# Performance work log

Hardware: AMD Instinct MI355X
Metric: run time of the kernel (lower is better)

Reference implementation:

```python
import jax, jax.numpy as jnp
import numpy as np
import math

D_MODEL = 1024
N_HEADS = 16
SLOT_DIM = 64
N_SLOTS = 1024
TOP_K = 2
LN_EPS = 1e-5


def setup_inputs() -> dict:
    key = jax.random.key(0)
    ks = jax.random.split(key, 8)
    x = jax.random.normal(ks[0], (4, 2048, D_MODEL), dtype=jnp.float32)
    ln_gamma = jnp.ones((D_MODEL,), jnp.float32)
    ln_beta = jnp.zeros((D_MODEL,), jnp.float32)
    q_w = jax.random.normal(ks[1], (N_HEADS * SLOT_DIM, D_MODEL), jnp.float32) / math.sqrt(D_MODEL)
    q_b = jnp.zeros((N_HEADS * SLOT_DIM,), jnp.float32)
    slot_signatures = jax.random.normal(ks[2], (N_HEADS, N_SLOTS, SLOT_DIM), jnp.float32) * 0.5
    slot_values = jax.random.normal(ks[3], (N_HEADS, N_SLOTS, SLOT_DIM), jnp.float32) * 0.02
    out_w = jax.random.normal(ks[4], (D_MODEL, N_HEADS * SLOT_DIM), jnp.float32) / math.sqrt(N_HEADS * SLOT_DIM)
    out_b = jnp.zeros((D_MODEL,), jnp.float32)
    temperature = jnp.ones((1,), jnp.float32)
    return {"x": x, "ln_gamma": ln_gamma, "ln_beta": ln_beta, "q_w": q_w, "q_b": q_b,
            "slot_signatures": slot_signatures, "slot_values": slot_values,
            "out_w": out_w, "out_b": out_b, "temperature": temperature}


def _ternary_ste(sig):
    # forward = {-1,0,+1} quantization; backward = identity (straight-through)
    q = jnp.where(sig > 0.3, 1.0, jnp.where(sig < -0.3, -1.0, 0.0))
    return sig + jax.lax.stop_gradient(q - sig)


def reference(x, ln_gamma, ln_beta, q_w, q_b, slot_signatures, slot_values, out_w, out_b, temperature):
    B, T, D = x.shape
    # LayerNorm
    mean = jnp.mean(x, axis=-1, keepdims=True)
    var = jnp.var(x, axis=-1, keepdims=True)
    x_norm = (x - mean) * jax.lax.rsqrt(var + LN_EPS) * ln_gamma + ln_beta
    # Query projection -> [B, T, H, slot_dim]
    q = (x_norm @ q_w.T + q_b).reshape(B, T, N_HEADS, SLOT_DIM)
    sigs = _ternary_ste(slot_signatures)  # [H, S, d]
    scores = jnp.einsum('bthd,hsd->bths', q, sigs)
    scores = scores / (temperature * math.sqrt(SLOT_DIM))  # [B, T, H, S]
    # top-k routing
    topk_scores, slot_idx = jax.lax.top_k(scores, TOP_K)  # [B, T, H, K]
    weights = jax.nn.softmax(topk_scores, axis=-1)
    # gather selected slot values: [B, T, H, K, d]
    h_idx = jnp.arange(N_HEADS)[None, None, :, None]
    selected = slot_values[h_idx, slot_idx]
    read = jnp.sum(selected * weights[..., None], axis=3)  # [B, T, H, d]
    read = read.reshape(B, T, N_HEADS * SLOT_DIM)
    out = read @ out_w.T + out_b
    return x + out
```

## Files before the change

kernel.cpp:

```cpp
#include <hip/hip_runtime.h>

typedef unsigned short u16;
typedef unsigned int   u32;
typedef float f32x4  __attribute__((ext_vector_type(4)));
typedef float f32x16 __attribute__((ext_vector_type(16)));
typedef __bf16 bf16x8 __attribute__((ext_vector_type(8)));

__device__ __forceinline__ u16 f2bf(float f){
  u32 u = __float_as_uint(f);
  u += 0x7fffu + ((u >> 16) & 1u);
  return (u16)(u >> 16);
}

__device__ __forceinline__ void gld16(const void* g, void* l){
  __builtin_amdgcn_global_load_lds((const __attribute__((address_space(1))) u32*)g,
                                   (__attribute__((address_space(3))) u32*)l, 16, 0, 0);
}

__global__ __launch_bounds__(256) void convert_kernel(
    const float* __restrict__ qw, const float* __restrict__ ow,
    const float* __restrict__ sg,
    u16* __restrict__ qwb, u16* __restrict__ owb, u16* __restrict__ sgb){
  int i = (blockIdx.x * 256 + threadIdx.x) * 4;
  f32x4 a = *(const f32x4*)(qw + i);
  f32x4 b = *(const f32x4*)(ow + i);
  f32x4 s = *(const f32x4*)(sg + i);
  uint2 pa, pb, ps;
  pa.x = (u32)f2bf(a[0]) | ((u32)f2bf(a[1]) << 16);
  pa.y = (u32)f2bf(a[2]) | ((u32)f2bf(a[3]) << 16);
  pb.x = (u32)f2bf(b[0]) | ((u32)f2bf(b[1]) << 16);
  pb.y = (u32)f2bf(b[2]) | ((u32)f2bf(b[3]) << 16);
  float t0 = (s[0] > 0.3f) ? 1.0f : ((s[0] < -0.3f) ? -1.0f : 0.0f);
  float t1 = (s[1] > 0.3f) ? 1.0f : ((s[1] < -0.3f) ? -1.0f : 0.0f);
  float t2 = (s[2] > 0.3f) ? 1.0f : ((s[2] < -0.3f) ? -1.0f : 0.0f);
  float t3 = (s[3] > 0.3f) ? 1.0f : ((s[3] < -0.3f) ? -1.0f : 0.0f);
  ps.x = (u32)f2bf(t0) | ((u32)f2bf(t1) << 16);
  ps.y = (u32)f2bf(t2) | ((u32)f2bf(t3) << 16);
  *(uint2*)(qwb + i) = pa;
  *(uint2*)(owb + i) = pb;
  *(uint2*)(sgb + i) = ps;
}

__global__ __launch_bounds__(256) void ln_kernel(
    const float* __restrict__ x, const float* __restrict__ g,
    const float* __restrict__ b, u16* __restrict__ xn){
  const int t = blockIdx.x, tid = threadIdx.x;
  f32x4 v = *(const f32x4*)(x + (size_t)t * 1024 + tid * 4);
  float s  = v[0] + v[1] + v[2] + v[3];
  float ss = v[0]*v[0] + v[1]*v[1] + v[2]*v[2] + v[3]*v[3];
  for (int off = 32; off; off >>= 1){
    s  += __shfl_down(s, off);
    ss += __shfl_down(ss, off);
  }
  __shared__ float red[8];
  int w = tid >> 6;
  if ((tid & 63) == 0){ red[w] = s; red[4 + w] = ss; }
  __syncthreads();
  s  = red[0] + red[1] + red[2] + red[3];
  ss = red[4] + red[5] + red[6] + red[7];
  float mean = s * (1.0f / 1024.0f);
  float var  = ss * (1.0f / 1024.0f) - mean * mean;
  float rs   = rsqrtf(var + 1e-5f);
  f32x4 gv = *(const f32x4*)(g + tid * 4);
  f32x4 bv = *(const f32x4*)(b + tid * 4);
  float y0 = (v[0]-mean)*rs*gv[0]+bv[0];
  float y1 = (v[1]-mean)*rs*gv[1]+bv[1];
  float y2 = (v[2]-mean)*rs*gv[2]+bv[2];
  float y3 = (v[3]-mean)*rs*gv[3]+bv[3];
  uint2 pk;
  pk.x = (u32)f2bf(y0) | ((u32)f2bf(y1) << 16);
  pk.y = (u32)f2bf(y2) | ((u32)f2bf(y3) << 16);
  *(uint2*)(xn + (size_t)t * 1024 + tid * 4) = pk;
}

__global__ __launch_bounds__(256, 3) void gemm_bt(
    const u16* __restrict__ A, const u16* __restrict__ B,
    const float* __restrict__ bias, const float* __restrict__ resid,
    float* __restrict__ outf, u16* __restrict__ outb, int mode){
  __shared__ u16 As[128 * 64];
  __shared__ u16 Bs[128 * 64];
  const int tid = threadIdx.x;
  const int b = blockIdx.x;
  const int m0 = ((b & 7) * 8 + ((b >> 3) & 7)) * 128;
  const int n0 = (b >> 6) * 128;
  const int w = tid >> 6, lane = tid & 63, lm = lane & 15, quad = lane >> 4;
  const int wm = (w & 1) * 64, wn = (w >> 1) * 64;
  const int lr = lane >> 3;
  const int lg = (lane & 7) ^ lr;
  const f32x4 fz = {0.f, 0.f, 0.f, 0.f};
  f32x4 acc[4][4];
  #pragma unroll
  for (int i = 0; i < 4; ++i)
    #pragma unroll
    for (int j = 0; j < 4; ++j) acc[i][j] = fz;

  const u16* gA = A + (size_t)(m0 + w * 32 + lr) * 1024 + lg * 8;
  const u16* gB = B + (size_t)(n0 + w * 32 + lr) * 1024 + lg * 8;
  u16* lA = &As[(w * 32) * 64];
  u16* lB = &Bs[(w * 32) * 64];
  const int sw = lm & 7;

  for (int kt = 0; kt < 16; ++kt){
    #pragma unroll
    for (int sub = 0; sub < 4; ++sub){
      gld16(gA + (size_t)(sub * 8) * 1024 + kt * 64, lA + sub * 8 * 64);
      gld16(gB + (size_t)(sub * 8) * 1024 + kt * 64, lB + sub * 8 * 64);
    }
    __syncthreads();
    #pragma unroll
    for (int kk = 0; kk < 2; ++kk){
      const int ch = ((quad + kk * 4) ^ sw) * 8;
      bf16x8 afr[4], bfr[4];
      #pragma unroll
      for (int i = 0; i < 4; ++i)
        afr[i] = *(const bf16x8*)(&As[(wm + i * 16 + lm) * 64 + ch]);
      #pragma unroll
      for (int j = 0; j < 4; ++j)
        bfr[j] = *(const bf16x8*)(&Bs[(wn + j * 16 + lm) * 64 + ch]);
      #pragma unroll
      for (int i = 0; i < 4; ++i)
        #pragma unroll
        for (int j = 0; j < 4; ++j)
          acc[i][j] = __builtin_amdgcn_mfma_f32_16x16x32_bf16(afr[i], bfr[j], acc[i][j], 0, 0, 0);
    }
    __syncthreads();
  }

  #pragma unroll
  for (int i = 0; i < 4; ++i){
    #pragma unroll
    for (int r = 0; r < 4; ++r){
      int grow = m0 + wm + i * 16 + quad * 4 + r;
      #pragma unroll
      for (int j = 0; j < 4; ++j){
        int gcol = n0 + wn + j * 16 + lm;
        float v = acc[i][j][r] + bias[gcol];
        if (mode){
          v += resid[(size_t)grow * 1024 + gcol];
          outf[(size_t)grow * 1024 + gcol] = v;
        } else {
          outb[(size_t)grow * 1024 + gcol] = f2bf(v);
        }
      }
    }
  }
}

__global__ __launch_bounds__(256) void route_kernel(
    const u16* __restrict__ q, const u16* __restrict__ sig,
    const float* __restrict__ V, const float* __restrict__ temp,
    u16* __restrict__ rd){
  const int h = blockIdx.y;
  const int t0 = blockIdx.x * 128;
  const int tid = threadIdx.x, w = tid >> 6, lane = tid & 63;
  const int col = lane & 31, half = lane >> 5;

  __shared__ u16 sbuf[2][128 * 64];
  __shared__ float fw1[128], fw2[128];
  __shared__ int   fi1[128], fi2[128];

  const u16* qrow = q + (size_t)(t0 + w * 32 + col) * 1024 + h * 64 + half * 8;
  bf16x8 afr[4];
  #pragma unroll
  for (int c = 0; c < 4; ++c) afr[c] = *(const bf16x8*)(qrow + c * 16);

  const u16* sigh = sig + (size_t)h * 65536;

  const int lr = lane >> 3, lg = (lane & 7) ^ lr;
  const u16* ssrc = sigh + (size_t)(w * 32 + lr) * 64 + lg * 8;
  auto stage = [&](int t, int bb){
    const u16* s0 = ssrc + (size_t)t * 128 * 64;
    u16* d0 = &sbuf[bb][(w * 32) * 64];
    #pragma unroll
    for (int sub = 0; sub < 4; ++sub)
      gld16(s0 + sub * 8 * 64, d0 + sub * 8 * 64);
  };

  int p0 = ((0 + half) ^ (col & 7)) * 8;
  int p1 = ((2 + half) ^ (col & 7)) * 8;
  int p2 = ((4 + half) ^ (col & 7)) * 8;
  int p3 = ((6 + half) ^ (col & 7)) * 8;

  u32 rk[16];
  #pragma unroll
  for (int r = 0; r < 16; ++r) rk[r] = (u32)((r & 3) + 8 * (r >> 2) + 4 * half);

  const f32x16 fzero = {};
  float v1 = -3.0e38f, v2 = -3.0e38f;
  u32 b1 = 0, b2 = 0;

  stage(0, 0);
  for (int t = 0; t < 8; ++t){
    __syncthreads();
    if (t < 7) stage(t + 1, (t + 1) & 1);
    const u16* buf = sbuf[t & 1];
    #pragma unroll
    for (int sbl = 0; sbl < 4; ++sbl){
      const u16* srow = &buf[(sbl * 32 + col) * 64];
      bf16x8 s0 = *(const bf16x8*)(srow + p0);
      bf16x8 s1 = *(const bf16x8*)(srow + p1);
      bf16x8 s2 = *(const bf16x8*)(srow + p2);
      bf16x8 s3 = *(const bf16x8*)(srow + p3);
      f32x16 acc;
      acc = __builtin_amdgcn_mfma_f32_32x32x16_bf16(s0, afr[0], fzero, 0, 0, 0);
      acc = __builtin_amdgcn_mfma_f32_32x32x16_bf16(s1, afr[1], acc, 0, 0, 0);
      acc = __builtin_amdgcn_mfma_f32_32x32x16_bf16(s2, afr[2], acc, 0, 0, 0);
      acc = __builtin_amdgcn_mfma_f32_32x32x16_bf16(s3, afr[3], acc, 0, 0, 0);
      float k[16];
      #pragma unroll
      for (int r = 0; r < 16; ++r)
        k[r] = __uint_as_float((__float_as_uint(acc[r]) & 0xFFFFFFE0u) | rk[r]);
      float h1[8], h2[8];
      #pragma unroll
      for (int i = 0; i < 8; ++i){
        h1[i] = fmaxf(k[2*i], k[2*i+1]);
        h2[i] = fminf(k[2*i], k[2*i+1]);
      }
      float g1[4], g2[4];
      #pragma unroll
      for (int i = 0; i < 4; ++i){
        g1[i] = fmaxf(h1[2*i], h1[2*i+1]);
        g2[i] = __builtin_amdgcn_fmed3f(h1[2*i], h1[2*i+1], fmaxf(h2[2*i], h2[2*i+1]));
      }
      float e1[2], e2[2];
      #pragma unroll
      for (int i = 0; i < 2; ++i){
        e1[i] = fmaxf(g1[2*i], g1[2*i+1]);
        e2[i] = __builtin_amdgcn_fmed3f(g1[2*i], g1[2*i+1], fmaxf(g2[2*i], g2[2*i+1]));
      }
      float m1 = fmaxf(e1[0], e1[1]);
      float m2 = __builtin_amdgcn_fmed3f(e1[0], e1[1], fmaxf(e2[0], e2[1]));
      u32 bt = (u32)(t * 4 + sbl);
      u32   cb2 = (m2 > v2) ? bt : b2;
      float c2  = fmaxf(v2, m2);
      u32   nb1 = (m1 > v1) ? bt : b1;
      float n1  = fmaxf(v1, m1);
      float n2  = __builtin_amdgcn_fmed3f(v1, m1, c2);
      u32   nb2 = (n2 == m1) ? bt : ((n2 == v1) ? b1 : cb2);
      v1 = n1; b1 = nb1; v2 = n2; b2 = nb2;
    }
  }

  {
    float o1 = __shfl_xor(v1, 32);
    float o2 = __shfl_xor(v2, 32);
    u32 ob1 = (u32)__shfl_xor((int)b1, 32);
    u32 ob2 = (u32)__shfl_xor((int)b2, 32);
    u32   cb2 = (o2 > v2) ? ob2 : b2;
    float c2  = fmaxf(v2, o2);
    u32   nb1 = (o1 > v1) ? ob1 : b1;
    float n1  = fmaxf(v1, o1);
    float n2  = __builtin_amdgcn_fmed3f(v1, o1, c2);
    u32   nb2 = (n2 == o1) ? ob1 : ((n2 == v1) ? b1 : cb2);
    v1 = n1; b1 = nb1; v2 = n2; b2 = nb2;
  }

  if (half == 0){
    int tl = w * 32 + col;
    u32 u1 = __float_as_uint(v1);
    u32 u2 = __float_as_uint(v2);
    float s1 = __uint_as_float(u1 & 0xFFFFFFE0u);
    float s2 = __uint_as_float(u2 & 0xFFFFFFE0u);
    float tsc = 1.0f / (temp[0] * 8.0f);
    float ex = __expf((s2 - s1) * tsc);
    float iw = 1.0f / (1.0f + ex);
    fw1[tl] = iw; fw2[tl] = ex * iw;
    fi1[tl] = (int)(b1 * 32 + (u1 & 31u));
    fi2[tl] = (int)(b2 * 32 + (u2 & 31u));
  }
  __syncthreads();

  int tl = tid >> 1, d0 = (tid & 1) * 32;
  const float* va = V + ((size_t)h * 1024 + fi1[tl]) * 64 + d0;
  const float* vb = V + ((size_t)h * 1024 + fi2[tl]) * 64 + d0;
  float W1 = fw1[tl], W2 = fw2[tl];
  u16* dst = rd + (size_t)(t0 + tl) * 1024 + h * 64 + d0;
  #pragma unroll
  for (int g = 0; g < 4; ++g){
    f32x4 xa = *(const f32x4*)(va + g * 8);
    f32x4 xb = *(const f32x4*)(va + g * 8 + 4);
    f32x4 ya = *(const f32x4*)(vb + g * 8);
    f32x4 yb = *(const f32x4*)(vb + g * 8 + 4);
    uint4 o;
    o.x = (u32)f2bf(W1*xa[0]+W2*ya[0]) | ((u32)f2bf(W1*xa[1]+W2*ya[1]) << 16);
    o.y = (u32)f2bf(W1*xa[2]+W2*ya[2]) | ((u32)f2bf(W1*xa[3]+W2*ya[3]) << 16);
    o.z = (u32)f2bf(W1*xb[0]+W2*yb[0]) | ((u32)f2bf(W1*xb[1]+W2*yb[1]) << 16);
    o.w = (u32)f2bf(W1*xb[2]+W2*yb[2]) | ((u32)f2bf(W1*xb[3]+W2*yb[3]) << 16);
    *(uint4*)(dst + g * 8) = o;
  }
}

extern "C" void kernel_launch(void* const* d_in, const int* in_sizes, int n_in,
                              void* d_out, int out_size, void* d_ws, size_t ws_size,
                              hipStream_t stream){
  const float* x    = (const float*)d_in[0];
  const float* lng  = (const float*)d_in[1];
  const float* lnb  = (const float*)d_in[2];
  const float* qw   = (const float*)d_in[3];
  const float* qb   = (const float*)d_in[4];
  const float* sig  = (const float*)d_in[5];
  const float* sv   = (const float*)d_in[6];
  const float* ow   = (const float*)d_in[7];
  const float* ob   = (const float*)d_in[8];
  const float* temp = (const float*)d_in[9];
  float* out = (float*)d_out;

  char* ws = (char*)d_ws;
  u16* xn   = (u16*)(ws);
  u16* qwb  = (u16*)(ws + 16777216);
  u16* owb  = (u16*)(ws + 16777216 + 2097152);
  u16* sgb  = (u16*)(ws + 16777216 + 2 * 2097152);
  u16* qb16 = (u16*)(ws + 16777216 + 3 * 2097152);
  u16* rdb  = xn;

  convert_kernel<<<1024, 256, 0, stream>>>(qw, ow, sig, qwb, owb, sgb);
  ln_kernel<<<8192, 256, 0, stream>>>(x, lng, lnb, xn);
  gemm_bt<<<512, 256, 0, stream>>>(xn, qwb, qb, nullptr, nullptr, qb16, 0);
  route_kernel<<<dim3(64, 16), 256, 0, stream>>>(qb16, sgb, sv, temp, rdb);
  gemm_bt<<<512, 256, 0, stream>>>(rdb, owb, ob, x, out, nullptr, 1);
}
```

Baseline: 211.7 us.

## Double-buffer GEMM LDS tiles and switch routing scores to 16x16 MFMA

The GEMM kernel now double-buffers its A/B LDS tiles, issuing the next K-tile's global-to-LDS loads before computing the current one and dropping the trailing barrier. This doubles LDS use and lowers the occupancy hint from 3 to 2 blocks. The routing kernel replaces its 32x32x16 MFMA score computation with 16x16x32 MFMAs over two token sets per wave. It packs a 4-bit slot index into the score mantissa instead of 5 bits and adds a two-stage shuffle reduction across quads. The aim is to hide load latency in the GEMM and shorten the top-2 reduction chain, at the cost of slightly more index-packing truncation of scores.

```diff
diff --git a/kernel.cpp b/kernel.cpp
--- a/kernel.cpp
+++ b/kernel.cpp
@@ -3,7 +3,6 @@
 typedef unsigned short u16;
 typedef unsigned int   u32;
 typedef float f32x4  __attribute__((ext_vector_type(4)));
-typedef float f32x16 __attribute__((ext_vector_type(16)));
 typedef __bf16 bf16x8 __attribute__((ext_vector_type(8)));
 
 __device__ __forceinline__ u16 f2bf(float f){
@@ -73,12 +72,12 @@
   *(uint2*)(xn + (size_t)t * 1024 + tid * 4) = pk;
 }
 
-__global__ __launch_bounds__(256, 3) void gemm_bt(
+__global__ __launch_bounds__(256, 2) void gemm_bt(
     const u16* __restrict__ A, const u16* __restrict__ B,
     const float* __restrict__ bias, const float* __restrict__ resid,
     float* __restrict__ outf, u16* __restrict__ outb, int mode){
-  __shared__ u16 As[128 * 64];
-  __shared__ u16 Bs[128 * 64];
+  __shared__ u16 As[2][128 * 64];
+  __shared__ u16 Bs[2][128 * 64];
   const int tid = threadIdx.x;
   const int b = blockIdx.x;
   const int m0 = ((b & 7) * 8 + ((b >> 3) & 7)) * 128;
@@ -96,34 +95,39 @@
 
   const u16* gA = A + (size_t)(m0 + w * 32 + lr) * 1024 + lg * 8;
   const u16* gB = B + (size_t)(n0 + w * 32 + lr) * 1024 + lg * 8;
-  u16* lA = &As[(w * 32) * 64];
-  u16* lB = &Bs[(w * 32) * 64];
+  const int lbase = (w * 32) * 64;
   const int sw = lm & 7;
 
+  auto stage = [&](int kt, int bb){
+    #pragma unroll
+    for (int sub = 0; sub < 4; ++sub){
+      gld16(gA + (size_t)(sub * 8) * 1024 + kt * 64, &As[bb][lbase + sub * 8 * 64]);
+      gld16(gB + (size_t)(sub * 8) * 1024 + kt * 64, &Bs[bb][lbase + sub * 8 * 64]);
+    }
+  };
+
+  stage(0, 0);
   for (int kt = 0; kt < 16; ++kt){
-    #pragma unroll
-    for (int sub = 0; sub < 4; ++sub){
-      gld16(gA + (size_t)(sub * 8) * 1024 + kt * 64, lA + sub * 8 * 64);
-      gld16(gB + (size_t)(sub * 8) * 1024 + kt * 64, lB + sub * 8 * 64);
-    }
     __syncthreads();
+    if (kt < 15) stage(kt + 1, (kt + 1) & 1);
+    const u16* as = As[kt & 1];
+    const u16* bs = Bs[kt & 1];
     #pragma unroll
     for (int kk = 0; kk < 2; ++kk){
       const int ch = ((quad + kk * 4) ^ sw) * 8;
       bf16x8 afr[4], bfr[4];
       #pragma unroll
       for (int i = 0; i < 4; ++i)
-        afr[i] = *(const bf16x8*)(&As[(wm + i * 16 + lm) * 64 + ch]);
+        afr[i] = *(const bf16x8*)(&as[(wm + i * 16 + lm) * 64 + ch]);
       #pragma unroll
       for (int j = 0; j < 4; ++j)
-        bfr[j] = *(const bf16x8*)(&Bs[(wn + j * 16 + lm) * 64 + ch]);
+        bfr[j] = *(const bf16x8*)(&bs[(wn + j * 16 + lm) * 64 + ch]);
       #pragma unroll
       for (int i = 0; i < 4; ++i)
         #pragma unroll
         for (int j = 0; j < 4; ++j)
           acc[i][j] = __builtin_amdgcn_mfma_f32_16x16x32_bf16(afr[i], bfr[j], acc[i][j], 0, 0, 0);
     }
-    __syncthreads();
   }
 
   #pragma unroll
@@ -153,16 +157,17 @@
   const int h = blockIdx.y;
   const int t0 = blockIdx.x * 128;
   const int tid = threadIdx.x, w = tid >> 6, lane = tid & 63;
-  const int col = lane & 31, half = lane >> 5;
+  const int lm = lane & 15, quad = lane >> 4;
 
   __shared__ u16 sbuf[2][128 * 64];
   __shared__ float fw1[128], fw2[128];
   __shared__ int   fi1[128], fi2[128];
 
-  const u16* qrow = q + (size_t)(t0 + w * 32 + col) * 1024 + h * 64 + half * 8;
-  bf16x8 afr[4];
-  #pragma unroll
-  for (int c = 0; c < 4; ++c) afr[c] = *(const bf16x8*)(qrow + c * 16);
+  const u16* q0 = q + (size_t)(t0 + w * 32 + lm) * 1024 + h * 64 + quad * 8;
+  bf16x8 qf00 = *(const bf16x8*)(q0);
+  bf16x8 qf01 = *(const bf16x8*)(q0 + 32);
+  bf16x8 qf10 = *(const bf16x8*)(q0 + 16 * 1024);
+  bf16x8 qf11 = *(const bf16x8*)(q0 + 16 * 1024 + 32);
 
   const u16* sigh = sig + (size_t)h * 65536;
 
@@ -176,18 +181,13 @@
       gld16(s0 + sub * 8 * 64, d0 + sub * 8 * 64);
   };
 
-  int p0 = ((0 + half) ^ (col & 7)) * 8;
-  int p1 = ((2 + half) ^ (col & 7)) * 8;
-  int p2 = ((4 + half) ^ (col & 7)) * 8;
-  int p3 = ((6 + half) ^ (col & 7)) * 8;
-
-  u32 rk[16];
-  #pragma unroll
-  for (int r = 0; r < 16; ++r) rk[r] = (u32)((r & 3) + 8 * (r >> 2) + 4 * half);
-
-  const f32x16 fzero = {};
-  float v1 = -3.0e38f, v2 = -3.0e38f;
-  u32 b1 = 0, b2 = 0;
+  const int base1 = lm * 64 + ((quad ^ (lm & 7)) * 8);
+  const int base2 = base1 ^ 32;
+
+  const f32x4 fz4 = {0.f, 0.f, 0.f, 0.f};
+  const u32 vq = (u32)(quad * 4);
+  float v1a = -3.0e38f, v2a = -3.0e38f, v1b = -3.0e38f, v2b = -3.0e38f;
+  u32 b1a = 0, b2a = 0, b1b = 0, b2b = 0;
 
   stage(0, 0);
   for (int t = 0; t < 8; ++t){
@@ -195,78 +195,74 @@
     if (t < 7) stage(t + 1, (t + 1) & 1);
     const u16* buf = sbuf[t & 1];
     #pragma unroll
-    for (int sbl = 0; sbl < 4; ++sbl){
-      const u16* srow = &buf[(sbl * 32 + col) * 64];
-      bf16x8 s0 = *(const bf16x8*)(srow + p0);
-      bf16x8 s1 = *(const bf16x8*)(srow + p1);
-      bf16x8 s2 = *(const bf16x8*)(srow + p2);
-      bf16x8 s3 = *(const bf16x8*)(srow + p3);
-      f32x16 acc;
-      acc = __builtin_amdgcn_mfma_f32_32x32x16_bf16(s0, afr[0], fzero, 0, 0, 0);
-      acc = __builtin_amdgcn_mfma_f32_32x32x16_bf16(s1, afr[1], acc, 0, 0, 0);
-      acc = __builtin_amdgcn_mfma_f32_32x32x16_bf16(s2, afr[2], acc, 0, 0, 0);
-      acc = __builtin_amdgcn_mfma_f32_32x32x16_bf16(s3, afr[3], acc, 0, 0, 0);
-      float k[16];
-      #pragma unroll
-      for (int r = 0; r < 16; ++r)
-        k[r] = __uint_as_float((__float_as_uint(acc[r]) & 0xFFFFFFE0u) | rk[r]);
-      float h1[8], h2[8];
-      #pragma unroll
-      for (int i = 0; i < 8; ++i){
-        h1[i] = fmaxf(k[2*i], k[2*i+1]);
-        h2[i] = fminf(k[2*i], k[2*i+1]);
+    for (int g = 0; g < 8; ++g){
+      bf16x8 s1 = *(const bf16x8*)(&buf[g * 1024 + base1]);
+      bf16x8 s2 = *(const bf16x8*)(&buf[g * 1024 + base2]);
+      u32 bt = (u32)(t * 8 + g);
+      #pragma unroll
+      for (int set = 0; set < 2; ++set){
+        f32x4 acc = __builtin_amdgcn_mfma_f32_16x16x32_bf16(s1, set ? qf10 : qf00, fz4, 0, 0, 0);
+        acc       = __builtin_amdgcn_mfma_f32_16x16x32_bf16(s2, set ? qf11 : qf01, acc, 0, 0, 0);
+        float k0 = __uint_as_float((__float_as_uint(acc[0]) & 0xFFFFFFF0u) | vq);
+        float k1 = __uint_as_float((__float_as_uint(acc[1]) & 0xFFFFFFF0u) | (vq + 1u));
+        float k2 = __uint_as_float((__float_as_uint(acc[2]) & 0xFFFFFFF0u) | (vq + 2u));
+        float k3 = __uint_as_float((__float_as_uint(acc[3]) & 0xFFFFFFF0u) | (vq + 3u));
+        float h1 = fmaxf(k0, k1), h2 = fminf(k0, k1);
+        float h3 = fmaxf(k2, k3), h4 = fminf(k2, k3);
+        float m1 = fmaxf(h1, h3);
+        float m2 = __builtin_amdgcn_fmed3f(h1, h3, fmaxf(h2, h4));
+        float v1 = set ? v1b : v1a, v2 = set ? v2b : v2a;
+        u32   b1 = set ? b1b : b1a, b2 = set ? b2b : b2a;
+        u32   cb2 = (m2 > v2) ? bt : b2;
+        float c2  = fmaxf(v2, m2);
+        u32   nb1 = (m1 > v1) ? bt : b1;
+        float n1  = fmaxf(v1, m1);
+        float n2  = __builtin_amdgcn_fmed3f(v1, m1, c2);
+        u32   nb2 = (n2 == m1) ? bt : ((n2 == v1) ? b1 : cb2);
+        if (set){ v1b = n1; b1b = nb1; v2b = n2; b2b = nb2; }
+        else    { v1a = n1; b1a = nb1; v2a = n2; b2a = nb2; }
       }
-      float g1[4], g2[4];
-      #pragma unroll
-      for (int i = 0; i < 4; ++i){
-        g1[i] = fmaxf(h1[2*i], h1[2*i+1]);
-        g2[i] = __builtin_amdgcn_fmed3f(h1[2*i], h1[2*i+1], fmaxf(h2[2*i], h2[2*i+1]));
-      }
-      float e1[2], e2[2];
-      #pragma unroll
-      for (int i = 0; i < 2; ++i){
-        e1[i] = fmaxf(g1[2*i], g1[2*i+1]);
-        e2[i] = __builtin_amdgcn_fmed3f(g1[2*i], g1[2*i+1], fmaxf(g2[2*i], g2[2*i+1]));
-      }
-      float m1 = fmaxf(e1[0], e1[1]);
-      float m2 = __builtin_amdgcn_fmed3f(e1[0], e1[1], fmaxf(e2[0], e2[1]));
-      u32 bt = (u32)(t * 4 + sbl);
-      u32   cb2 = (m2 > v2) ? bt : b2;
-      float c2  = fmaxf(v2, m2);
-      u32   nb1 = (m1 > v1) ? bt : b1;
-      float n1  = fmaxf(v1, m1);
-      float n2  = __builtin_amdgcn_fmed3f(v1, m1, c2);
-      u32   nb2 = (n2 == m1) ? bt : ((n2 == v1) ? b1 : cb2);
-      v1 = n1; b1 = nb1; v2 = n2; b2 = nb2;
-    }
-  }
-
-  {
-    float o1 = __shfl_xor(v1, 32);
-    float o2 = __shfl_xor(v2, 32);
-    u32 ob1 = (u32)__shfl_xor((int)b1, 32);
-    u32 ob2 = (u32)__shfl_xor((int)b2, 32);
-    u32   cb2 = (o2 > v2) ? ob2 : b2;
-    float c2  = fmaxf(v2, o2);
-    u32   nb1 = (o1 > v1) ? ob1 : b1;
-    float n1  = fmaxf(v1, o1);
-    float n2  = __builtin_amdgcn_fmed3f(v1, o1, c2);
-    u32   nb2 = (n2 == o1) ? ob1 : ((n2 == v1) ? b1 : cb2);
-    v1 = n1; b1 = nb1; v2 = n2; b2 = nb2;
-  }
-
-  if (half == 0){
-    int tl = w * 32 + col;
-    u32 u1 = __float_as_uint(v1);
-    u32 u2 = __float_as_uint(v2);
-    float s1 = __uint_as_float(u1 & 0xFFFFFFE0u);
-    float s2 = __uint_as_float(u2 & 0xFFFFFFE0u);
+    }
+  }
+
+  #pragma unroll
+  for (int off = 16; off <= 32; off <<= 1){
+    #pragma unroll
+    for (int set = 0; set < 2; ++set){
+      float v1 = set ? v1b : v1a, v2 = set ? v2b : v2a;
+      u32   b1 = set ? b1b : b1a, b2 = set ? b2b : b2a;
+      float o1 = __shfl_xor(v1, off);
+      float o2 = __shfl_xor(v2, off);
+      u32 ob1 = (u32)__shfl_xor((int)b1, off);
+      u32 ob2 = (u32)__shfl_xor((int)b2, off);
+      u32   cb2 = (o2 > v2) ? ob2 : b2;
+      float c2  = fmaxf(v2, o2);
+      u32   nb1 = (o1 > v1) ? ob1 : b1;
+      float n1  = fmaxf(v1, o1);
+      float n2  = __builtin_amdgcn_fmed3f(v1, o1, c2);
+      u32   nb2 = (n2 == o1) ? ob1 : ((n2 == v1) ? b1 : cb2);
+      if (set){ v1b = n1; b1b = nb1; v2b = n2; b2b = nb2; }
+      else    { v1a = n1; b1a = nb1; v2a = n2; b2a = nb2; }
+    }
+  }
+
+  if (quad == 0){
     float tsc = 1.0f / (temp[0] * 8.0f);
-    float ex = __expf((s2 - s1) * tsc);
-    float iw = 1.0f / (1.0f + ex);
-    fw1[tl] = iw; fw2[tl] = ex * iw;
-    fi1[tl] = (int)(b1 * 32 + (u1 & 31u));
-    fi2[tl] = (int)(b2 * 32 + (u2 & 31u));
+    #pragma unroll
+    for (int set = 0; set < 2; ++set){
+      float v1 = set ? v1b : v1a, v2 = set ? v2b : v2a;
+      u32   b1 = set ? b1b : b1a, b2 = set ? b2b : b2a;
+      int tl = w * 32 + set * 16 + lm;
+      u32 u1 = __float_as_uint(v1);
+      u32 u2 = __float_as_uint(v2);
+      float s1 = __uint_as_float(u1 & 0xFFFFFFF0u);
+      float s2 = __uint_as_float(u2 & 0xFFFFFFF0u);
+      float ex = __expf((s2 - s1) * tsc);
+      float iw = 1.0f / (1.0f + ex);
+      fw1[tl] = iw; fw2[tl] = ex * iw;
+      fi1[tl] = (int)(b1 * 16 + (u1 & 15u));
+      fi2[tl] = (int)(b2 * 16 + (u2 & 15u));
+    }
   }
   __syncthreads();
 
```

Measured after the change: 217.1 us. +2.6%, slower.
